# Performance work log

Measured on AMD Instinct MI355X. Metric: run time of the kernel, lower is better.

## Reference

```python
import jax, jax.numpy as jnp
import numpy as np

NY = NX = 512
DX = DY = 200.0
RHO, G, FD = 910.0, 9.81, 1e-16
TTOT, DTMAX = 200.0, 1.0
EPS = 1e-10
T_FREQ = 5.0
LAPSE = 0.006        # degC per m, lapse rate used by assumed update_smb
MELT = 0.5           # m/yr per degC, degree-day melt factor
N_STEPS = 400        # fixed upper bound on while-loop iterations (dt<=1yr, ttot=200yr)
N_PRECIP = 64


def _make_squash(scale):
    # identity in forward; backward applies atan(scale*g)/scale (torch register_hook)
    @jax.custom_vjp
    def f(x):
        return x
    def fwd(x):
        return x, None
    def bwd(_, g):
        return (jnp.arctan(scale * g) / scale,)
    f.defvjp(fwd, bwd)
    return f

squash_smb = _make_squash(0.51)   # reduce_hook
squash_zs = _make_squash(0.051)   # reduce_hook2


def update_smb(Z_surf, precip, T_m_lowest, T_s):
    # degree-day surface mass balance (update_smb not present in source excerpt)
    T = T_m_lowest[0] + T_s[0] - LAPSE * Z_surf
    return precip - MELT * jnp.maximum(T, 0.0)


def setup_inputs() -> dict:
    key = jax.random.key(0)
    k1, = jax.random.split(key, 1)
    # smooth synthetic mountain topography (Gaussian bump, 3000 m peak)
    y = np.linspace(-1.0, 1.0, NY, dtype=np.float32)
    x = np.linspace(-1.0, 1.0, NX, dtype=np.float32)
    xx, yy = np.meshgrid(x, y)
    Z_topo = jnp.asarray(3000.0 * np.exp(-(xx ** 2 + yy ** 2) / 0.3), dtype=jnp.float32)
    precip_tensor = 2.0 * jax.random.uniform(k1, (N_PRECIP, NY, NX), dtype=jnp.float32)
    T_m_lowest = jnp.array([5.0], dtype=jnp.float32)
    T_s = jnp.array([2.0], dtype=jnp.float32)
    return {"Z_topo": Z_topo, "precip_tensor": precip_tensor,
            "T_m_lowest": T_m_lowest, "T_s": T_s}


def _solve(Z_topo, precip_tensor, T_m_lowest, T_s):
    H = jnp.zeros((NY, NX), jnp.float32)
    Zs = Z_topo + H
    smb = update_smb(Zs, precip_tensor[0], T_m_lowest, T_s)
    zero2d = jnp.zeros((NY, NX), jnp.float32)
    carry0 = (H, Zs, smb, jnp.float32(0.0), jnp.int32(0), jnp.float32(0.0),
              zero2d, zero2d, jnp.bool_(False), jnp.bool_(False))

    def step(carry, _):
        H, Zs, smb, time, idx, t_last, H1, H2, s1, s2 = carry
        active = time < TTOT
        # staggered-grid SIA stencil
        H_avg = 0.25 * (H[:-1, :-1] + H[1:, 1:] + H[:-1, 1:] + H[1:, :-1])
        Sx = (Zs[:, 1:] - Zs[:, :-1]) / DX
        Sy = (Zs[1:, :] - Zs[:-1, :]) / DY
        Sx = 0.5 * (Sx[:-1, :] + Sx[1:, :])
        Sy = 0.5 * (Sy[:, :-1] + Sy[:, 1:])
        Snorm = jnp.sqrt(Sx ** 2 + Sy ** 2 + EPS)
        D = FD * (RHO * G) ** 3 * H_avg ** 5 * Snorm ** 2 + EPS   # (ny-1, nx-1)
        # dt via .item() in torch -> detached constant
        dt = jax.lax.stop_gradient(
            jnp.minimum(min(DX, DY) ** 2 / (2.7 * jnp.max(D)), DTMAX))
        dt = jnp.where(active, dt, jnp.float32(0.0))  # no-op once ttot reached
        qx = -(0.5 * (D[:-1, :] + D[1:, :])) * (Zs[1:-1, 1:] - Zs[1:-1, :-1]) / DX
        qy = -(0.5 * (D[:, :-1] + D[:, 1:])) * (Zs[1:, 1:-1] - Zs[:-1, 1:-1]) / DY
        dHdt = -(jnp.diff(qx, axis=1) / DX + jnp.diff(qy, axis=0) / DY)  # (ny-2, nx-2)
        smb_sq = squash_smb(smb)
        H = H.at[1:-1, 1:-1].add(dt * (dHdt + smb_sq[1:-1, 1:-1]))
        H = jax.nn.relu(H)
        Zs = squash_zs(Z_topo + H)
        time = time + dt
        cap1 = jnp.logical_and(jnp.logical_not(s1), time >= 120.0)
        H1 = jnp.where(cap1, jax.lax.stop_gradient(H), H1)
        s1 = jnp.logical_or(s1, cap1)
        cap2 = jnp.logical_and(jnp.logical_not(s2), time >= 160.0)
        H2 = jnp.where(cap2, jax.lax.stop_gradient(H), H2)
        s2 = jnp.logical_or(s2, cap2)
        do_upd = jnp.logical_and(active, (time - t_last) >= T_FREQ)
        idx = jnp.where(do_upd, jnp.minimum(idx + 1, N_PRECIP - 1), idx)
        smb_new = update_smb(Zs, precip_tensor[idx], T_m_lowest, T_s)
        smb = jnp.where(do_upd, smb_new, smb)
        t_last = jnp.where(do_upd, time, t_last)
        return (H, Zs, smb, time, idx, t_last, H1, H2, s1, s2), None

    carry, _ = jax.lax.scan(jax.checkpoint(step), carry0, None, length=N_STEPS)
    H, Zs, smb, time, idx, t_last, H1, H2, s1, s2 = carry
    return H1, H2, H


def reference(Z_topo, precip_tensor, T_m_lowest, T_s):
    return _solve(Z_topo, precip_tensor, T_m_lowest, T_s)
```

## Files before the change

### kernel.cpp

```cpp
#include <hip/hip_runtime.h>
#include <math.h>


#define NN 512
#define MM (NN * NN)
#define NSTEPS 400
#define NW 128
#define HR 4
#define TPB 512

typedef unsigned long long ull;

__device__ __forceinline__ ull ald(const ull* p) {
  return __hip_atomic_load(p, __ATOMIC_RELAXED, __HIP_MEMORY_SCOPE_AGENT);
}
__device__ __forceinline__ void asto(ull* p, ull v) {
  __hip_atomic_store(p, v, __ATOMIC_RELAXED, __HIP_MEMORY_SCOPE_AGENT);
}

__global__ __launch_bounds__(TPB)
void glacier_kernel(const float* __restrict__ Zt,
                    const float* __restrict__ precip,
                    const float* __restrict__ Tm,
                    const float* __restrict__ Ts,
                    float* __restrict__ out,
                    ull* __restrict__ ring,
                    ull* __restrict__ halo) {
  __shared__ float Zs2[2][HR + 4][NN];
  __shared__ float DB[HR + 3][NN];
  __shared__ float HnB[HR + 2][NN];
  __shared__ float gmax2[2];
  __shared__ unsigned lmx[2], lcnt[2];

  ull* upH = halo;
  ull* upD = halo + 2 * NW * NN;
  ull* dnH = halo + 4 * NW * NN;
  ull* dnD = halo + 6 * NW * NN;

  const int w = blockIdx.x;
  const int j = threadIdx.x;
  const int lane = j & 63;
  const int a = w * HR;
  const bool hasT = (w > 0), hasB = (w < NW - 1);
  const float TmTs = Tm[0] + Ts[0];
  const double RG = 910.0 * 9.81;
  const float CDIF = (float)(1e-16 * RG * RG * RG);
  const float C_Q = 1.25e-5f;
  const float C_S2 = 6.25e-6f;
  const size_t wofs = (size_t)w * NN;

  float ztreg[HR + 4];
  float hcur[HR + 2];
  float smbreg[HR + 2];

#pragma unroll
  for (int ls = 0; ls < HR + 4; ++ls) {
    int r = a - 2 + ls;
    float zt = (r >= 0 && r < NN) ? Zt[r * NN + j] : 0.f;
    ztreg[ls] = zt;
    Zs2[0][ls][j] = zt;
  }
#pragma unroll
  for (int ln = 0; ln < HR + 2; ++ln) {
    int r = a - 1 + ln;
    hcur[ln] = 0.f;
    float sm = 0.f;
    if (r >= 0 && r < NN) {
      float T = TmTs - 0.006f * ztreg[ln + 1];
      sm = precip[r * NN + j] - 0.5f * fmaxf(T, 0.f);
    }
    smbreg[ln] = sm;
  }
#pragma unroll
  for (int ld = 0; ld < HR + 3; ++ld) DB[ld][j] = 1e-10f;
#pragma unroll
  for (int rr = 0; rr < HR; ++rr) {
    int id = (a + rr) * NN + j;
    out[id] = 0.f;
    out[MM + id] = 0.f;
  }
  if (j == 0) { lmx[0] = 0u; lmx[1] = 0u; lcnt[0] = 0u; lcnt[1] = 0u; }
  __syncthreads();

  float time = 0.f, t_last = 0.f;
  int idx = 0;
  bool s1 = false, s2 = false;

  for (int k = 0; k < NSTEPS; ++k) {
    if (time >= 200.0f) break;

    const int p = k & 1;
    const size_t pc = (size_t)(k & 1) * NW * NN;
    const size_t pn = (size_t)((k + 1) & 1) * NW * NN;
    const ull tg = ((ull)(unsigned)(k + 1)) << 32;
    ull* ringp = ring + (size_t)(k & 1) * NW * 16;

    if (j == 0) { lmx[(k + 1) & 1] = 0u; lcnt[(k + 1) & 1] = 0u; }

    bool pre = (time - t_last) >= 4.0f;
    int idxn = min(idx + 1, 63);
    float pf[HR + 2];
    if (pre) {
      const float* prowN = precip + (size_t)idxn * MM;
#pragma unroll
      for (int ln = 0; ln < HR + 2; ++ln) {
        int i = a - 1 + ln;
        pf[ln] = (i >= 0 && i < NN) ? prowN[i * NN + j] : 0.f;
      }
    } else {
#pragma unroll
      for (int ln = 0; ln < HR + 2; ++ln) pf[ln] = 0.f;
    }
    const ull *pHt = nullptr, *pDt = nullptr, *pHb = nullptr, *pDb = nullptr;
    ull vHt = 0, vDt = 0, vHb = 0, vDb = 0;
    const ull* gp = nullptr; ull gv = 0;
    if (k > 0) {
      if (hasT) {
        pHt = dnH + pc + (size_t)(w - 1) * NN + j;
        pDt = dnD + pc + (size_t)(w - 1) * NN + j;
        vHt = ald(pHt);
        if (j < NN - 1) vDt = ald(pDt);
      }
      if (hasB) {
        pHb = upH + pc + (size_t)(w + 1) * NN + j;
        pDb = upD + pc + (size_t)(w + 1) * NN + j;
        vHb = ald(pHb);
        if (j < NN - 1) vDb = ald(pDb);
      }
      if (j < NW) { gp = ringp + j * 16; gv = ald(gp); }
    }
    asm volatile("" ::: "memory");

    float dHdt[HR + 2];
#pragma unroll
    for (int ln = 1; ln <= HR; ++ln) {
      int i = a - 1 + ln;
      float v = 0.f;
      if (i > 0 && i < NN - 1 && j > 0 && j < NN - 1) {
        int li = ln + 1;
        float zc = Zs2[p][li][j];
        float zw = Zs2[p][li][j - 1];
        float ze = Zs2[p][li][j + 1];
        float zn = Zs2[p][li - 1][j];
        float zs_ = Zs2[p][li + 1][j];
        float d00 = DB[ln][j - 1], d01 = DB[ln][j];
        float d10 = DB[ln + 1][j - 1], d11 = DB[ln + 1][j];
        v = C_Q * (((d01 + d11) * (ze - zc) - (d00 + d10) * (zc - zw)) +
                   ((d10 + d11) * (zs_ - zc) - (d00 + d01) * (zc - zn)));
      }
      dHdt[ln] = v;
    }

    if (k > 0) {
      if (pHt) {
        while ((unsigned)(vHt >> 32) < (unsigned)k) {
          __builtin_amdgcn_s_sleep(1); vHt = ald(pHt);
        }
        if (j < NN - 1)
          while ((unsigned)(vDt >> 32) < (unsigned)k) {
            __builtin_amdgcn_s_sleep(1); vDt = ald(pDt);
          }
      }
      if (pHb) {
        while ((unsigned)(vHb >> 32) < (unsigned)k) {
          __builtin_amdgcn_s_sleep(1); vHb = ald(pHb);
        }
        if (j < NN - 1)
          while ((unsigned)(vDb >> 32) < (unsigned)k) {
            __builtin_amdgcn_s_sleep(1); vDb = ald(pDb);
          }
      }
      if (j < NW) {
        while ((unsigned)(gv >> 32) < (unsigned)k) {
          __builtin_amdgcn_s_sleep(1); gv = ald(gp);
        }
        float lm = __uint_as_float((unsigned)gv);
        for (int off = 32; off; off >>= 1) lm = fmaxf(lm, __shfl_xor(lm, off));
        if (lane == 0) gmax2[j >> 6] = lm;
      }
      if (pHt) {
        Zs2[p][0][j] = ztreg[0] + __uint_as_float((unsigned)vHt);
        if (j < NN - 1) DB[0][j] = __uint_as_float((unsigned)vDt);
      }
      if (pHb) {
        Zs2[p][HR + 3][j] = ztreg[HR + 3] + __uint_as_float((unsigned)vHb);
        if (j < NN - 1) DB[HR + 2][j] = __uint_as_float((unsigned)vDb);
      }
    }
    __syncthreads();

#pragma unroll
    for (int ln = 0; ln <= HR + 1; ln += HR + 1) {
      int i = a - 1 + ln;
      float v = 0.f;
      if (i > 0 && i < NN - 1 && j > 0 && j < NN - 1) {
        int li = ln + 1;
        float zc = Zs2[p][li][j];
        float zw = Zs2[p][li][j - 1];
        float ze = Zs2[p][li][j + 1];
        float zn = Zs2[p][li - 1][j];
        float zs_ = Zs2[p][li + 1][j];
        float d00 = DB[ln][j - 1], d01 = DB[ln][j];
        float d10 = DB[ln + 1][j - 1], d11 = DB[ln + 1][j];
        v = C_Q * (((d01 + d11) * (ze - zc) - (d00 + d10) * (zc - zw)) +
                   ((d10 + d11) * (zs_ - zc) - (d00 + d01) * (zc - zn)));
      }
      dHdt[ln] = v;
    }

    float maxD = (k == 0) ? 1e-10f : fmaxf(gmax2[0], gmax2[1]);
    float dt = fminf(40000.0f / (2.7f * maxD), 1.0f);
    float tnew = time + dt;
    bool cap1 = (!s1) && (tnew >= 120.0f);
    bool cap2 = (!s2) && (tnew >= 160.0f);
    bool do_upd = (tnew - t_last) >= 5.0f;

    float hnxt[HR + 2];
#pragma unroll
    for (int ln = 0; ln < HR + 2; ++ln) {
      int i = a - 1 + ln;
      float hnew = 0.f;
      if (i >= 0 && i < NN) {
        if (i > 0 && i < NN - 1 && j > 0 && j < NN - 1)
          hnew = fmaxf(hcur[ln] + dt * (dHdt[ln] + smbreg[ln]), 0.f);
        float zsn = ztreg[ln + 1] + hnew;
        HnB[ln][j] = hnew;
        Zs2[p ^ 1][ln + 1][j] = zsn;
        if (ln == 2) asto(upH + pn + wofs + j, tg | (ull)__float_as_uint(hnew));
        if (ln == 3) asto(dnH + pn + wofs + j, tg | (ull)__float_as_uint(hnew));
        if (i >= a && i < a + HR) {
          int id = i * NN + j;
          if (cap1) out[id] = hnew;
          if (cap2) out[MM + id] = hnew;
        }
        if (do_upd)
          smbreg[ln] = pf[ln] - 0.5f * fmaxf(TmTs - 0.006f * zsn, 0.f);
      }
      hnxt[ln] = hnew;
    }
    __syncthreads();

    float lmax = 0.f;
#pragma unroll
    for (int ln = 0; ln < HR + 1; ++ln) {
      int r = a - 1 + ln;
      if (r >= 0 && r < NN - 1 && j < NN - 1) {
        float h00 = HnB[ln][j], h01 = HnB[ln][j + 1];
        float h10 = HnB[ln + 1][j], h11 = HnB[ln + 1][j + 1];
        float z00 = Zs2[p ^ 1][ln + 1][j], z01 = Zs2[p ^ 1][ln + 1][j + 1];
        float z10 = Zs2[p ^ 1][ln + 2][j], z11 = Zs2[p ^ 1][ln + 2][j + 1];
        float havg = 0.25f * (((h00 + h11) + h01) + h10);
        float u = (z01 - z00) + (z11 - z10);
        float vv = (z10 - z00) + (z11 - z01);
        float s2 = C_S2 * (u * u + vv * vv) + 1e-10f;
        float h2 = havg * havg;
        float h4 = h2 * h2;
        float h5 = h4 * havg;
        float d = CDIF * h5 * s2 + 1e-10f;
        DB[ln + 1][j] = d;
        if (ln == 1) asto(upD + pn + wofs + j, tg | (ull)__float_as_uint(d));
        if (ln == 3) asto(dnD + pn + wofs + j, tg | (ull)__float_as_uint(d));
        lmax = fmaxf(lmax, d);
      }
    }
    for (int off = 32; off; off >>= 1) lmax = fmaxf(lmax, __shfl_xor(lmax, off));
    if (lane == 0) {
      atomicMax(&lmx[k & 1], __float_as_uint(lmax));
      unsigned c = atomicAdd(&lcnt[k & 1], 1u);
      if (c == 7u) {
        unsigned mv = atomicAdd(&lmx[k & 1], 0u);
        asto(ring + (size_t)((k + 1) & 1) * NW * 16 + w * 16,
             ((ull)(unsigned)(k + 1) << 32) | (ull)mv);
      }
    }

#pragma unroll
    for (int ln = 0; ln < HR + 2; ++ln) hcur[ln] = hnxt[ln];
    time = tnew;
    s1 = s1 || cap1;
    s2 = s2 || cap2;
    if (do_upd) { idx = idxn; t_last = tnew; }
    __syncthreads();
  }

#pragma unroll
  for (int rr = 0; rr < HR; ++rr)
    out[2 * MM + (a + rr) * NN + j] = hcur[rr + 1];
}

extern "C" void kernel_launch(void* const* d_in, const int* in_sizes, int n_in,
                              void* d_out, int out_size, void* d_ws, size_t ws_size,
                              hipStream_t stream) {
  const float* Zt = (const float*)d_in[0];
  const float* precip = (const float*)d_in[1];
  const float* Tm = (const float*)d_in[2];
  const float* Ts = (const float*)d_in[3];
  float* out = (float*)d_out;

  ull* ring = (ull*)d_ws;
  ull* halo = (ull*)((char*)d_ws + 32768);

  hipMemsetAsync(d_ws, 0, 32768 + (size_t)8 * NW * NN * sizeof(ull), stream);
  glacier_kernel<<<NW, TPB, 0, stream>>>(Zt, precip, Tm, Ts, out, ring, halo);
}
```

Measured before the change: 1.276 ms.

## Defer global max-D wait past the barrier using tagged LDS mailbox

The spin-wait on the global maximum diffusivity moves from before the block barrier to after it. The result is published through a tagged 64-bit shared-memory slot that other waves poll only when they need dt. Boundary dHdt rows and the dHdt+smb sums are computed while the global reduction is still arriving, and the update becomes an fma. This aims to overlap the cross-block latency with local compute, at the cost of LDS spin-polling and a subtle ordering dependency.

```diff
diff --git a/kernel.cpp b/kernel.cpp
--- a/kernel.cpp
+++ b/kernel.cpp
@@ -16,6 +16,12 @@
 }
 __device__ __forceinline__ void asto(ull* p, ull v) {
   __hip_atomic_store(p, v, __ATOMIC_RELAXED, __HIP_MEMORY_SCOPE_AGENT);
+}
+__device__ __forceinline__ ull lld(const ull* p) {
+  return __hip_atomic_load(p, __ATOMIC_RELAXED, __HIP_MEMORY_SCOPE_WORKGROUP);
+}
+__device__ __forceinline__ void lst(ull* p, ull v) {
+  __hip_atomic_store(p, v, __ATOMIC_RELAXED, __HIP_MEMORY_SCOPE_WORKGROUP);
 }
 
 __global__ __launch_bounds__(TPB)
@@ -29,7 +35,7 @@
   __shared__ float Zs2[2][HR + 4][NN];
   __shared__ float DB[HR + 3][NN];
   __shared__ float HnB[HR + 2][NN];
-  __shared__ float gmax2[2];
+  __shared__ ull gm[2];
   __shared__ unsigned lmx[2], lcnt[2];
 
   ull* upH = halo;
@@ -79,7 +85,8 @@
     out[id] = 0.f;
     out[MM + id] = 0.f;
   }
-  if (j == 0) { lmx[0] = 0u; lmx[1] = 0u; lcnt[0] = 0u; lcnt[1] = 0u; }
+  if (j == 0) { lmx[0] = 0u; lmx[1] = 0u; lcnt[0] = 0u; lcnt[1] = 0u;
+                gm[0] = 0ull; gm[1] = 0ull; }
   __syncthreads();
 
   float time = 0.f, t_last = 0.f;
@@ -170,14 +177,6 @@
             __builtin_amdgcn_s_sleep(1); vDb = ald(pDb);
           }
       }
-      if (j < NW) {
-        while ((unsigned)(gv >> 32) < (unsigned)k) {
-          __builtin_amdgcn_s_sleep(1); gv = ald(gp);
-        }
-        float lm = __uint_as_float((unsigned)gv);
-        for (int off = 32; off; off >>= 1) lm = fmaxf(lm, __shfl_xor(lm, off));
-        if (lane == 0) gmax2[j >> 6] = lm;
-      }
       if (pHt) {
         Zs2[p][0][j] = ztreg[0] + __uint_as_float((unsigned)vHt);
         if (j < NN - 1) DB[0][j] = __uint_as_float((unsigned)vDt);
@@ -188,6 +187,16 @@
       }
     }
     __syncthreads();
+
+    if (k > 0 && j < NW) {
+      while ((unsigned)(gv >> 32) < (unsigned)k) {
+        __builtin_amdgcn_s_sleep(1); gv = ald(gp);
+      }
+      float lm = __uint_as_float((unsigned)gv);
+      for (int off = 32; off; off >>= 1) lm = fmaxf(lm, __shfl_xor(lm, off));
+      if (lane == 0)
+        lst(&gm[j >> 6], ((ull)(unsigned)k << 32) | (ull)__float_as_uint(lm));
+    }
 
 #pragma unroll
     for (int ln = 0; ln <= HR + 1; ln += HR + 1) {
@@ -208,7 +217,25 @@
       dHdt[ln] = v;
     }
 
-    float maxD = (k == 0) ? 1e-10f : fmaxf(gmax2[0], gmax2[1]);
+    float sd[HR + 2];
+#pragma unroll
+    for (int ln = 0; ln < HR + 2; ++ln) sd[ln] = dHdt[ln] + smbreg[ln];
+
+    float maxD;
+    if (k == 0) {
+      maxD = 1e-10f;
+    } else {
+      ull g0 = lld(&gm[0]);
+      while ((unsigned)(g0 >> 32) < (unsigned)k) {
+        __builtin_amdgcn_s_sleep(1); g0 = lld(&gm[0]);
+      }
+      ull g1 = lld(&gm[1]);
+      while ((unsigned)(g1 >> 32) < (unsigned)k) {
+        __builtin_amdgcn_s_sleep(1); g1 = lld(&gm[1]);
+      }
+      maxD = fmaxf(__uint_as_float((unsigned)g0),
+                   __uint_as_float((unsigned)g1));
+    }
     float dt = fminf(40000.0f / (2.7f * maxD), 1.0f);
     float tnew = time + dt;
     bool cap1 = (!s1) && (tnew >= 120.0f);
@@ -222,7 +249,7 @@
       float hnew = 0.f;
       if (i >= 0 && i < NN) {
         if (i > 0 && i < NN - 1 && j > 0 && j < NN - 1)
-          hnew = fmaxf(hcur[ln] + dt * (dHdt[ln] + smbreg[ln]), 0.f);
+          hnew = fmaxf(fmaf(dt, sd[ln], hcur[ln]), 0.f);
         float zsn = ztreg[ln + 1] + hnew;
         HnB[ln][j] = hnew;
         Zs2[p ^ 1][ln + 1][j] = zsn;
```

After: 1.269 ms, median of 2. Within noise of the previous version (-0.5%).
